# Optimization experiments

Hardware: AMD Instinct MI355X
Metric: run time of the kernel (lower is better)

Reference implementation:

```python
import jax, jax.numpy as jnp
import numpy as np

N = 50000      # nodes per graph
E = 1600000    # edges per graph
D_IN = 128
D_HID = 128
D_OUT = 128
D_GF = 128
N_LAYERS = 3   # input->hid, hid->hid (hidden_layer=1), hid->out


def setup_inputs() -> dict:
    key = jax.random.key(0)
    ks = jax.random.split(key, 24)
    inp = {
        "feat_p": jax.random.normal(ks[0], (N, D_IN), jnp.float32),
        "src_p": jax.random.randint(ks[1], (E,), 0, N, jnp.int32),
        "dst_p": jax.random.randint(ks[2], (E,), 0, N, jnp.int32),
        "feat_s": jax.random.normal(ks[3], (N, D_IN), jnp.float32),
        "src_s": jax.random.randint(ks[4], (E,), 0, N, jnp.int32),
        "dst_s": jax.random.randint(ks[5], (E,), 0, N, jnp.int32),
    }
    dims = [(D_IN, D_HID), (D_HID, D_HID), (D_HID, D_OUT)]
    for i, (di, do) in enumerate(dims):
        inp[f"W{i}"] = jax.random.normal(ks[6 + 2 * i], (di, do), jnp.float32) * 0.05
        inp[f"b{i}"] = jnp.zeros((do,), jnp.float32)
    inp["Wr"] = jax.random.normal(ks[14], (D_OUT, D_GF), jnp.float32) * 0.05
    inp["br"] = jnp.zeros((D_GF,), jnp.float32)
    inp["Wm1"] = jax.random.normal(ks[15], (2 * D_GF, D_GF), jnp.float32) * 0.05
    inp["bm1"] = jnp.zeros((D_GF,), jnp.float32)
    inp["Wm2"] = jax.random.normal(ks[16], (D_GF, 1), jnp.float32) * 0.05
    inp["bm2"] = jnp.zeros((1,), jnp.float32)
    return inp


def _gcn_stack(feat, src, dst, layers):
    """Stacked GCN: mean over incoming messages, then linear.
    NOTE: the original SingleGCN never applies its ReLU (bug preserved)."""
    n = feat.shape[0]
    deg = jax.ops.segment_sum(jnp.ones_like(src, feat.dtype), dst, num_segments=n)
    inv_deg = (1.0 / jnp.maximum(deg, 1.0))[:, None]  # [N,1]
    h = feat
    for W, b in layers:
        msg = h[src]                                           # [E,d] gather
        agg = jax.ops.segment_sum(msg, dst, num_segments=n)    # [N,d] scatter-add
        h = (agg * inv_deg) @ W + b                            # mean + linear
    return h


def reference(feat_p, src_p, dst_p, feat_s, src_s, dst_s,
              W0, b0, W1, b1, W2, b2, Wr, br, Wm1, bm1, Wm2, bm2):
    layers = [(W0, b0), (W1, b1), (W2, b2)]
    h_p = _gcn_stack(feat_p, src_p, dst_p, layers)
    h_s = _gcn_stack(feat_s, src_s, dst_s, layers)
    # ReadOut: mean over nodes -> linear -> sigmoid
    g_p = jax.nn.sigmoid(jnp.mean(h_p, axis=0) @ Wr + br)  # [D_GF]
    g_s = jax.nn.sigmoid(jnp.mean(h_s, axis=0) @ Wr + br)
    # Match: concat -> linear -> linear -> sigmoid
    c = jnp.concatenate([g_p, g_s], axis=-1)               # [2*D_GF]
    d = (c @ Wm1 + bm1) @ Wm2 + bm2                        # [1]
    return jax.nn.sigmoid(d)
```

## Files before the change

kernel.cpp:

```cpp
#include <hip/hip_runtime.h>
#include <math.h>

#define D 128
#define BSH 9
#define NPB 512
#define SLOT 128
#define STCAP 6252
#define NBB 256
#define NBKT_MAX 128
#define SB 8
#define CPS (NBB / SB)


__global__ __launch_bounds__(512) void bin_kernel(
        const int* __restrict__ src_p, const int* __restrict__ dst_p,
        const int* __restrict__ src_s, const int* __restrict__ dst_s,
        int* __restrict__ sbins, unsigned short* __restrict__ dbins,
        unsigned* __restrict__ cnt_s, unsigned* __restrict__ cnt_d,
        int E, int nbkt) {
    const int g = blockIdx.y, b = blockIdx.x;
    const int* src = g ? src_s : src_p;
    const int* dst = g ? dst_s : dst_p;
    int* sb = sbins + (size_t)g * nbkt * NBB * SLOT;
    unsigned short* db = dbins + (size_t)g * nbkt * NBB * SLOT;
    unsigned* csp = cnt_s + (size_t)g * nbkt * NBB;
    unsigned* cdp = cnt_d + (size_t)g * nbkt * NBB;

    __shared__ int sstage[STCAP];
    __shared__ unsigned short dstage[STCAP];
    __shared__ unsigned hist_s[NBKT_MAX], hist_d[NBKT_MAX];
    __shared__ unsigned offs_s[NBKT_MAX], offs_d[NBKT_MAX];
    __shared__ unsigned lcur_s[NBKT_MAX], lcur_d[NBKT_MAX];

    const int tid = threadIdx.x;
    const int wv = tid >> 6, lane = tid & 63;
    for (int i = tid; i < NBKT_MAX; i += 512) { hist_s[i] = 0u; hist_d[i] = 0u; }
    __syncthreads();

    const int e0 = b * STCAP;
    const int e1 = min(e0 + STCAP, E);
    const int efull = e0 + ((e1 - e0) & ~3);

    for (int e = e0 + tid * 4; e + 4 <= e1; e += 512 * 4) {
        int4 s4 = *(const int4*)(src + e);
        int4 d4 = *(const int4*)(dst + e);
        atomicAdd(&hist_s[s4.x >> BSH], 1u);
        atomicAdd(&hist_s[s4.y >> BSH], 1u);
        atomicAdd(&hist_s[s4.z >> BSH], 1u);
        atomicAdd(&hist_s[s4.w >> BSH], 1u);
        atomicAdd(&hist_d[d4.x >> BSH], 1u);
        atomicAdd(&hist_d[d4.y >> BSH], 1u);
        atomicAdd(&hist_d[d4.z >> BSH], 1u);
        atomicAdd(&hist_d[d4.w >> BSH], 1u);
    }
    for (int e = efull + tid; e < e1; e += 512) {
        atomicAdd(&hist_s[src[e] >> BSH], 1u);
        atomicAdd(&hist_d[dst[e] >> BSH], 1u);
    }
    __syncthreads();

    if (wv == 0 || wv == 1) {
        const unsigned* h = (wv == 0) ? hist_s : hist_d;
        unsigned* o = (wv == 0) ? offs_s : offs_d;
        unsigned* lc = (wv == 0) ? lcur_s : lcur_d;
        unsigned a = (2 * lane < nbkt) ? h[2 * lane] : 0u;
        unsigned bb = (2 * lane + 1 < nbkt) ? h[2 * lane + 1] : 0u;
        unsigned v = a + bb;
        for (int d2 = 1; d2 < 64; d2 <<= 1) {
            unsigned t = __shfl_up(v, d2);
            if (lane >= d2) v += t;
        }
        unsigned ex = v - (a + bb);
        if (2 * lane < nbkt) { o[2 * lane] = ex; lc[2 * lane] = ex; }
        if (2 * lane + 1 < nbkt) { o[2 * lane + 1] = ex + a; lc[2 * lane + 1] = ex + a; }
    }
    __syncthreads();

    for (int e = e0 + tid * 4; e + 4 <= e1; e += 512 * 4) {
        int4 s4 = *(const int4*)(src + e);
        int4 d4 = *(const int4*)(dst + e);
        int sv[4] = {s4.x, s4.y, s4.z, s4.w};
        int dv[4] = {d4.x, d4.y, d4.z, d4.w};
        #pragma unroll
        for (int k = 0; k < 4; ++k) {
            unsigned p = atomicAdd(&lcur_s[sv[k] >> BSH], 1u);
            sstage[p] = ((sv[k] & (NPB - 1)) << 17) | dv[k];
            unsigned pd = atomicAdd(&lcur_d[dv[k] >> BSH], 1u);
            dstage[pd] = (unsigned short)(dv[k] & (NPB - 1));
        }
    }
    for (int e = efull + tid; e < e1; e += 512) {
        int s = src[e], d2 = dst[e];
        unsigned p = atomicAdd(&lcur_s[s >> BSH], 1u);
        sstage[p] = ((s & (NPB - 1)) << 17) | d2;
        unsigned pd = atomicAdd(&lcur_d[d2 >> BSH], 1u);
        dstage[pd] = (unsigned short)(d2 & (NPB - 1));
    }
    __syncthreads();

    for (int q = wv; q < nbkt; q += 8) {
        unsigned cs = min(hist_s[q], (unsigned)SLOT);
        unsigned os = offs_s[q];
        int* dp = sb + ((size_t)q * NBB + b) * SLOT;
        for (unsigned i = lane; i < cs; i += 64) dp[i] = sstage[os + i];
        unsigned cd = min(hist_d[q], (unsigned)SLOT);
        unsigned od = offs_d[q];
        unsigned short* ddp = db + ((size_t)q * NBB + b) * SLOT;
        for (unsigned i = lane; i < cd; i += 64) ddp[i] = dstage[od + i];
        if (lane == 0) { csp[q * NBB + b] = cs; cdp[q * NBB + b] = cd; }
    }
}

__global__ __launch_bounds__(256) void deg_part(
        const unsigned short* __restrict__ dbins, const unsigned* __restrict__ cnt_d,
        float* __restrict__ partials, int nbkt) {
    const int s = blockIdx.x, q = blockIdx.y, g = blockIdx.z;
    const unsigned short* dq = dbins + ((size_t)(g * nbkt + q) * NBB + s * CPS) * SLOT;
    const unsigned* cq = cnt_d + (size_t)(g * nbkt + q) * NBB + s * CPS;
    const int tid = threadIdx.x, wv = tid >> 6;
    __shared__ float bl[4][NPB];
    __shared__ unsigned lcnt[CPS];
    if (tid < CPS) lcnt[tid] = cq[tid];
    for (int i = tid; i < 4 * NPB; i += 256) ((float*)bl)[i] = 0.f;
    __syncthreads();
    float* mybl = bl[wv];
    const ushort4* d4 = (const ushort4*)dq;
    const int total = CPS * (SLOT / 4);
    for (int i = tid; i < total; i += 256) {
        int lim = (int)lcnt[i >> 5] - ((i & 31) << 2);
        if (lim <= 0) continue;
        ushort4 v = d4[i];
        atomicAdd(&mybl[v.x], 1.f);
        if (lim > 1) atomicAdd(&mybl[v.y], 1.f);
        if (lim > 2) atomicAdd(&mybl[v.z], 1.f);
        if (lim > 3) atomicAdd(&mybl[v.w], 1.f);
    }
    __syncthreads();
    float* pp = partials + (((size_t)(g * nbkt + q)) * SB + s) * NPB;
    for (int i = tid; i < NPB; i += 256)
        pp[i] = bl[0][i] + bl[1][i] + bl[2][i] + bl[3][i];
}

__global__ __launch_bounds__(512) void deg_combine(
        const float* __restrict__ partials, float* __restrict__ inv,
        float* __restrict__ zbase, int zcount, int N, int nbkt) {
    const int q = blockIdx.x, g = blockIdx.y;
    const int tid = threadIdx.x;
    if (q == 0 && g == 0)
        for (int i = tid; i < zcount; i += 512) zbase[i] = 0.f;
    const float* pp = partials + ((size_t)(g * nbkt + q)) * SB * NPB;
    float t = 0.f;
    #pragma unroll
    for (int s = 0; s < SB; ++s) t += pp[s * NPB + tid];
    const int node = q * NPB + tid;
    if (node < N) inv[(size_t)g * N + node] = 1.0f / fmaxf(t, 1.0f);
}

__global__ __launch_bounds__(256) void part_scan(
        const int* __restrict__ sbins, const unsigned* __restrict__ cnt_s,
        const float* __restrict__ w, float* __restrict__ partials,
        int N, int nbkt) {
    const int s = blockIdx.x, q = blockIdx.y, g = blockIdx.z;
    const int* sq = sbins + ((size_t)(g * nbkt + q) * NBB + s * CPS) * SLOT;
    const unsigned* cq = cnt_s + (size_t)(g * nbkt + q) * NBB + s * CPS;
    const float* wg = w + (size_t)g * N;
    const int tid = threadIdx.x, wv = tid >> 6;
    __shared__ float bl[4][NPB];
    __shared__ unsigned lcnt[CPS];
    if (tid < CPS) lcnt[tid] = cq[tid];
    for (int i = tid; i < 4 * NPB; i += 256) ((float*)bl)[i] = 0.f;
    __syncthreads();
    float* mybl = bl[wv];
    const int4* s4 = (const int4*)sq;
    const int total = CPS * (SLOT / 4);
    for (int i = tid; i < total; i += 256) {
        int lim = (int)lcnt[i >> 5] - ((i & 31) << 2);
        if (lim <= 0) continue;
        int4 v = s4[i];
        int iy = (lim > 1) ? (v.y & 0x1FFFF) : 0;
        int iz = (lim > 2) ? (v.z & 0x1FFFF) : 0;
        int iw = (lim > 3) ? (v.w & 0x1FFFF) : 0;
        float a = wg[v.x & 0x1FFFF];
        float b2 = wg[iy];
        float c2 = wg[iz];
        float d2 = wg[iw];
        atomicAdd(&mybl[((unsigned)v.x) >> 17], a);
        if (lim > 1) atomicAdd(&mybl[((unsigned)v.y) >> 17], b2);
        if (lim > 2) atomicAdd(&mybl[((unsigned)v.z) >> 17], c2);
        if (lim > 3) atomicAdd(&mybl[((unsigned)v.w) >> 17], d2);
    }
    __syncthreads();
    float* pp = partials + (((size_t)(g * nbkt + q)) * SB + s) * NPB;
    for (int i = tid; i < NPB; i += 256)
        pp[i] = bl[0][i] + bl[1][i] + bl[2][i] + bl[3][i];
}

__global__ __launch_bounds__(512) void prop_combine(
        const float* __restrict__ partials, const float* __restrict__ inv,
        float* __restrict__ out_w, float* __restrict__ sums, int s_idx,
        int N, int nbkt, float scale) {
    const int q = blockIdx.x, g = blockIdx.y;
    const int tid = threadIdx.x;
    const float* pp = partials + ((size_t)(g * nbkt + q)) * SB * NPB;
    float t = 0.f;
    #pragma unroll
    for (int s = 0; s < SB; ++s) t += pp[s * NPB + tid];
    const float u = t * scale;
    const int node = q * NPB + tid;
    const bool valid = node < N;
    if (valid) {
        size_t off = (size_t)g * N + node;
        out_w[off] = u * inv[off];
    }
    __shared__ float red[NPB];
    red[tid] = valid ? u : 0.f;
    __syncthreads();
    for (int st = 256; st > 0; st >>= 1) {
        if (tid < st) red[tid] += red[tid + st];
        __syncthreads();
    }
    if (tid == 0 && red[0] != 0.f) atomicAdd(&sums[g * 2 + s_idx], red[0]);
}

__global__ __launch_bounds__(512) void feat_combine(
        const float* __restrict__ partials,
        const float* __restrict__ feat_p, const float* __restrict__ feat_s,
        float* __restrict__ fpart2, int N, int nbkt) {
    const int r = blockIdx.x, q = blockIdx.y, g = blockIdx.z;
    const int tid = threadIdx.x;
    __shared__ float red[256];
    __shared__ float accb[512];
    const float* pp = partials + ((size_t)(g * nbkt + q)) * SB * NPB + r * 256;
    const int base = q * NPB + r * 256;
    if (tid < 256) {
        float t = 0.f;
        #pragma unroll
        for (int s = 0; s < SB; ++s) t += pp[s * NPB + tid];
        red[tid] = (base + tid < N) ? t : 0.f;
    }
    __syncthreads();
    const float* feat = g ? feat_s : feat_p;
    const int j = tid & 127, rg = tid >> 7;
    int rmax = N - base;
    rmax = (rmax < 0) ? 0 : ((rmax > 256) ? 256 : rmax);
    const int rstart = rg * 64;
    const int rend = min(rstart + 64, rmax);
    float acc = 0.f;
    for (int row = rstart; row < rend; ++row)
        acc += red[row] * feat[(size_t)(base + row) * D + j];
    accb[rg * 128 + j] = acc;
    __syncthreads();
    if (rg == 0) {
        float tot = accb[j] + accb[128 + j] + accb[256 + j] + accb[384 + j];
        if (tot != 0.f)
            atomicAdd(&fpart2[((size_t)g * 16 + (q & 15)) * D + j], tot);
    }
}

__global__ __launch_bounds__(512) void final_kernel(
        const float* __restrict__ fpart2,
        const float* __restrict__ sums,
        const float* __restrict__ W0, const float* __restrict__ b0,
        const float* __restrict__ W1, const float* __restrict__ b1,
        const float* __restrict__ W2, const float* __restrict__ b2,
        const float* __restrict__ Wr, const float* __restrict__ br,
        const float* __restrict__ Wm1, const float* __restrict__ bm1,
        const float* __restrict__ Wm2, const float* __restrict__ bm2,
        float* __restrict__ out) {
    __shared__ float x[128];
    __shared__ float part[4][128];
    __shared__ float rvec[256];
    __shared__ float Avec[128], Bvec[128];
    __shared__ float gv[256];
    const int tid = threadIdx.x;
    const int j = tid & 127;
    const int h = tid >> 7;

    auto mv128 = [&](const float* __restrict__ W, float* __restrict__ buf) {
        float p = 0.f;
        const float* Wp = W + (size_t)(h * 32) * 128 + j;
        #pragma unroll
        for (int i = 0; i < 32; ++i) p += buf[h * 32 + i] * Wp[(size_t)i * 128];
        part[h][j] = p;
        __syncthreads();
        if (h == 0) buf[j] = part[0][j] + part[1][j] + part[2][j] + part[3][j];
        __syncthreads();
    };

    if (tid < 256) {
        int g = tid >> 7;
        const float* fp = fpart2 + (size_t)g * 2048 + (tid & 127);
        float rv = 0.f;
        #pragma unroll
        for (int b = 0; b < 16; ++b) rv += fp[(size_t)b * 128];
        rvec[tid] = rv;
    }
    __syncthreads();

    if (tid < 128) x[tid] = b0[tid];
    __syncthreads();
    mv128(W1, x);
    mv128(W2, x);
    if (tid < 128) Avec[tid] = x[tid];
    __syncthreads();
    if (tid < 128) x[tid] = b1[tid];
    __syncthreads();
    mv128(W2, x);
    if (tid < 128) Bvec[tid] = x[tid];
    __syncthreads();

    for (int g = 0; g < 2; ++g) {
        const float s1 = sums[g * 2 + 0];
        const float s2 = sums[g * 2 + 1];
        if (tid < 128) x[tid] = rvec[g * 128 + tid];
        __syncthreads();
        mv128(W0, x);
        mv128(W1, x);
        mv128(W2, x);
        if (tid < 128) x[tid] += s2 * Avec[tid] + s1 * Bvec[tid] + b2[tid];
        __syncthreads();
        mv128(Wr, x);
        if (tid < 128) gv[g * 128 + tid] = 1.0f / (1.0f + expf(-(x[tid] + br[tid])));
        __syncthreads();
    }

    {
        float p = 0.f;
        const float* Wp = Wm1 + (size_t)(h * 64) * 128 + j;
        #pragma unroll
        for (int i = 0; i < 64; ++i) p += gv[h * 64 + i] * Wp[(size_t)i * 128];
        part[h][j] = p;
        __syncthreads();
        if (h == 0)
            part[0][j] = (part[0][j] + part[1][j] + part[2][j] + part[3][j] + bm1[j]) * Wm2[j];
        __syncthreads();
        if (tid < 64) part[0][tid] += part[0][tid + 64];
        __syncthreads();
        if (tid < 32) part[0][tid] += part[0][tid + 32];
        __syncthreads();
        if (tid < 16) part[0][tid] += part[0][tid + 16];
        __syncthreads();
        if (tid < 8) part[0][tid] += part[0][tid + 8];
        __syncthreads();
        if (tid < 4) part[0][tid] += part[0][tid + 4];
        __syncthreads();
        if (tid < 2) part[0][tid] += part[0][tid + 2];
        __syncthreads();
        if (tid == 0) out[0] = 1.0f / (1.0f + expf(-(part[0][0] + part[0][1] + bm2[0])));
    }
}

extern "C" void kernel_launch(void* const* d_in, const int* in_sizes, int n_in,
                              void* d_out, int out_size, void* d_ws, size_t ws_size,
                              hipStream_t stream) {
    const float* feat_p = (const float*)d_in[0];
    const int*   src_p  = (const int*)d_in[1];
    const int*   dst_p  = (const int*)d_in[2];
    const float* feat_s = (const float*)d_in[3];
    const int*   src_s  = (const int*)d_in[4];
    const int*   dst_s  = (const int*)d_in[5];
    const float* W0 = (const float*)d_in[6];
    const float* b0 = (const float*)d_in[7];
    const float* W1 = (const float*)d_in[8];
    const float* b1 = (const float*)d_in[9];
    const float* W2 = (const float*)d_in[10];
    const float* b2 = (const float*)d_in[11];
    const float* Wr = (const float*)d_in[12];
    const float* br = (const float*)d_in[13];
    const float* Wm1 = (const float*)d_in[14];
    const float* bm1 = (const float*)d_in[15];
    const float* Wm2 = (const float*)d_in[16];
    const float* bm2 = (const float*)d_in[17];
    float* out = (float*)d_out;

    const int N = in_sizes[0] / D;
    const int E = in_sizes[1];
    const int N2 = 2 * N;
    const int nbkt = (N + NPB - 1) >> BSH;

    float* ws     = (float*)d_ws;
    float* sums   = ws;
    float* fpart2 = ws + 16;
    float* inv    = fpart2 + 2 * 16 * 128;
    float* w1     = inv + N2;
    float* w2     = w1 + N2;
    float* partials = w2 + N2;
    unsigned* cnt_s = (unsigned*)(partials + (size_t)2 * nbkt * SB * NPB);
    unsigned* cnt_d = cnt_s + (size_t)2 * nbkt * NBB;
    int* sbins    = (int*)(cnt_d + (size_t)2 * nbkt * NBB);
    unsigned short* dbins = (unsigned short*)(sbins + (size_t)2 * nbkt * NBB * SLOT);

    const float u0 = 1.0f / (float)N;
    const int zcount = 16 + 2 * 16 * 128;

    bin_kernel<<<dim3(NBB, 2), 512, 0, stream>>>(src_p, dst_p, src_s, dst_s,
                                                 sbins, dbins, cnt_s, cnt_d,
                                                 E, nbkt);

    deg_part<<<dim3(SB, nbkt, 2), 256, 0, stream>>>(dbins, cnt_d, partials, nbkt);
    deg_combine<<<dim3(nbkt, 2), 512, 0, stream>>>(partials, inv, ws, zcount,
                                                   N, nbkt);

    part_scan<<<dim3(SB, nbkt, 2), 256, 0, stream>>>(sbins, cnt_s, inv,
                                                     partials, N, nbkt);
    prop_combine<<<dim3(nbkt, 2), 512, 0, stream>>>(partials, inv, w1,
                                                    sums, 0, N, nbkt, u0);

    part_scan<<<dim3(SB, nbkt, 2), 256, 0, stream>>>(sbins, cnt_s, w1,
                                                     partials, N, nbkt);
    prop_combine<<<dim3(nbkt, 2), 512, 0, stream>>>(partials, inv, w2,
                                                    sums, 1, N, nbkt, 1.0f);

    part_scan<<<dim3(SB, nbkt, 2), 256, 0, stream>>>(sbins, cnt_s, w2,
                                                     partials, N, nbkt);
    feat_combine<<<dim3(2, nbkt, 2), 512, 0, stream>>>(partials, feat_p, feat_s,
                                                       fpart2, N, nbkt);

    final_kernel<<<1, 512, 0, stream>>>(fpart2, sums, W0, b0, W1, b1, W2, b2,
                                        Wr, br, Wm1, bm1, Wm2, bm2, out);
}
```

Baseline: 300.8 us.

## Split binning by key side, widen scan blocks, parallelize feat and final kernels

The binning kernel now runs separate blocks for src-keyed and dst-keyed binning, doubling grid parallelism and halving shared staging per block. The partial-scan and degree kernels use 512 threads with SB reduced to 4, batching loads ahead of the shared atomics to raise memory-level parallelism. feat_combine is split across 8 row chunks with float4 loads and a tree reduction into 32 accumulator slots. final_kernel processes both graphs concurrently with 1024 threads. The risk is extra passes over src/dst and more global atomics in feat_combine.

```diff
diff --git a/kernel.cpp b/kernel.cpp
--- a/kernel.cpp
+++ b/kernel.cpp
@@ -8,7 +8,7 @@
 #define STCAP 6252
 #define NBB 256
 #define NBKT_MAX 128
-#define SB 8
+#define SB 4
 #define CPS (NBB / SB)
 
 
@@ -18,23 +18,17 @@
         int* __restrict__ sbins, unsigned short* __restrict__ dbins,
         unsigned* __restrict__ cnt_s, unsigned* __restrict__ cnt_d,
         int E, int nbkt) {
-    const int g = blockIdx.y, b = blockIdx.x;
+    const int b = blockIdx.x, side = blockIdx.y, g = blockIdx.z;
     const int* src = g ? src_s : src_p;
     const int* dst = g ? dst_s : dst_p;
-    int* sb = sbins + (size_t)g * nbkt * NBB * SLOT;
-    unsigned short* db = dbins + (size_t)g * nbkt * NBB * SLOT;
-    unsigned* csp = cnt_s + (size_t)g * nbkt * NBB;
-    unsigned* cdp = cnt_d + (size_t)g * nbkt * NBB;
-
-    __shared__ int sstage[STCAP];
-    __shared__ unsigned short dstage[STCAP];
-    __shared__ unsigned hist_s[NBKT_MAX], hist_d[NBKT_MAX];
-    __shared__ unsigned offs_s[NBKT_MAX], offs_d[NBKT_MAX];
-    __shared__ unsigned lcur_s[NBKT_MAX], lcur_d[NBKT_MAX];
+    const int* key = side ? dst : src;
+
+    __shared__ int stage[STCAP];
+    __shared__ unsigned hist[NBKT_MAX], offs[NBKT_MAX], lcur[NBKT_MAX];
 
     const int tid = threadIdx.x;
     const int wv = tid >> 6, lane = tid & 63;
-    for (int i = tid; i < NBKT_MAX; i += 512) { hist_s[i] = 0u; hist_d[i] = 0u; }
+    for (int i = tid; i < NBKT_MAX; i += 512) hist[i] = 0u;
     __syncthreads();
 
     const int e0 = b * STCAP;
@@ -42,103 +36,124 @@
     const int efull = e0 + ((e1 - e0) & ~3);
 
     for (int e = e0 + tid * 4; e + 4 <= e1; e += 512 * 4) {
-        int4 s4 = *(const int4*)(src + e);
-        int4 d4 = *(const int4*)(dst + e);
-        atomicAdd(&hist_s[s4.x >> BSH], 1u);
-        atomicAdd(&hist_s[s4.y >> BSH], 1u);
-        atomicAdd(&hist_s[s4.z >> BSH], 1u);
-        atomicAdd(&hist_s[s4.w >> BSH], 1u);
-        atomicAdd(&hist_d[d4.x >> BSH], 1u);
-        atomicAdd(&hist_d[d4.y >> BSH], 1u);
-        atomicAdd(&hist_d[d4.z >> BSH], 1u);
-        atomicAdd(&hist_d[d4.w >> BSH], 1u);
-    }
-    for (int e = efull + tid; e < e1; e += 512) {
-        atomicAdd(&hist_s[src[e] >> BSH], 1u);
-        atomicAdd(&hist_d[dst[e] >> BSH], 1u);
-    }
-    __syncthreads();
-
-    if (wv == 0 || wv == 1) {
-        const unsigned* h = (wv == 0) ? hist_s : hist_d;
-        unsigned* o = (wv == 0) ? offs_s : offs_d;
-        unsigned* lc = (wv == 0) ? lcur_s : lcur_d;
-        unsigned a = (2 * lane < nbkt) ? h[2 * lane] : 0u;
-        unsigned bb = (2 * lane + 1 < nbkt) ? h[2 * lane + 1] : 0u;
+        int4 k4 = *(const int4*)(key + e);
+        atomicAdd(&hist[k4.x >> BSH], 1u);
+        atomicAdd(&hist[k4.y >> BSH], 1u);
+        atomicAdd(&hist[k4.z >> BSH], 1u);
+        atomicAdd(&hist[k4.w >> BSH], 1u);
+    }
+    for (int e = efull + tid; e < e1; e += 512)
+        atomicAdd(&hist[key[e] >> BSH], 1u);
+    __syncthreads();
+
+    if (wv == 0) {
+        unsigned a = (2 * lane < nbkt) ? hist[2 * lane] : 0u;
+        unsigned bb = (2 * lane + 1 < nbkt) ? hist[2 * lane + 1] : 0u;
         unsigned v = a + bb;
         for (int d2 = 1; d2 < 64; d2 <<= 1) {
             unsigned t = __shfl_up(v, d2);
             if (lane >= d2) v += t;
         }
         unsigned ex = v - (a + bb);
-        if (2 * lane < nbkt) { o[2 * lane] = ex; lc[2 * lane] = ex; }
-        if (2 * lane + 1 < nbkt) { o[2 * lane + 1] = ex + a; lc[2 * lane + 1] = ex + a; }
-    }
-    __syncthreads();
-
-    for (int e = e0 + tid * 4; e + 4 <= e1; e += 512 * 4) {
-        int4 s4 = *(const int4*)(src + e);
-        int4 d4 = *(const int4*)(dst + e);
-        int sv[4] = {s4.x, s4.y, s4.z, s4.w};
-        int dv[4] = {d4.x, d4.y, d4.z, d4.w};
-        #pragma unroll
-        for (int k = 0; k < 4; ++k) {
-            unsigned p = atomicAdd(&lcur_s[sv[k] >> BSH], 1u);
-            sstage[p] = ((sv[k] & (NPB - 1)) << 17) | dv[k];
-            unsigned pd = atomicAdd(&lcur_d[dv[k] >> BSH], 1u);
-            dstage[pd] = (unsigned short)(dv[k] & (NPB - 1));
-        }
-    }
-    for (int e = efull + tid; e < e1; e += 512) {
-        int s = src[e], d2 = dst[e];
-        unsigned p = atomicAdd(&lcur_s[s >> BSH], 1u);
-        sstage[p] = ((s & (NPB - 1)) << 17) | d2;
-        unsigned pd = atomicAdd(&lcur_d[d2 >> BSH], 1u);
-        dstage[pd] = (unsigned short)(d2 & (NPB - 1));
-    }
-    __syncthreads();
-
-    for (int q = wv; q < nbkt; q += 8) {
-        unsigned cs = min(hist_s[q], (unsigned)SLOT);
-        unsigned os = offs_s[q];
-        int* dp = sb + ((size_t)q * NBB + b) * SLOT;
-        for (unsigned i = lane; i < cs; i += 64) dp[i] = sstage[os + i];
-        unsigned cd = min(hist_d[q], (unsigned)SLOT);
-        unsigned od = offs_d[q];
-        unsigned short* ddp = db + ((size_t)q * NBB + b) * SLOT;
-        for (unsigned i = lane; i < cd; i += 64) ddp[i] = dstage[od + i];
-        if (lane == 0) { csp[q * NBB + b] = cs; cdp[q * NBB + b] = cd; }
-    }
-}
-
-__global__ __launch_bounds__(256) void deg_part(
+        if (2 * lane < nbkt) { offs[2 * lane] = ex; lcur[2 * lane] = ex; }
+        if (2 * lane + 1 < nbkt) { offs[2 * lane + 1] = ex + a; lcur[2 * lane + 1] = ex + a; }
+    }
+    __syncthreads();
+
+    if (side == 0) {
+        for (int e = e0 + tid * 4; e + 4 <= e1; e += 512 * 4) {
+            int4 s4 = *(const int4*)(src + e);
+            int4 d4 = *(const int4*)(dst + e);
+            int sv[4] = {s4.x, s4.y, s4.z, s4.w};
+            int dv[4] = {d4.x, d4.y, d4.z, d4.w};
+            #pragma unroll
+            for (int k = 0; k < 4; ++k) {
+                unsigned p = atomicAdd(&lcur[sv[k] >> BSH], 1u);
+                stage[p] = ((sv[k] & (NPB - 1)) << 17) | dv[k];
+            }
+        }
+        for (int e = efull + tid; e < e1; e += 512) {
+            int s = src[e], d2 = dst[e];
+            unsigned p = atomicAdd(&lcur[s >> BSH], 1u);
+            stage[p] = ((s & (NPB - 1)) << 17) | d2;
+        }
+        __syncthreads();
+        int* sb = sbins + (size_t)g * nbkt * NBB * SLOT;
+        unsigned* csp = cnt_s + (size_t)g * nbkt * NBB;
+        for (int q = wv; q < nbkt; q += 8) {
+            unsigned cs = min(hist[q], (unsigned)SLOT);
+            unsigned os = offs[q];
+            int* dp = sb + ((size_t)q * NBB + b) * SLOT;
+            for (unsigned i = lane; i < cs; i += 64) dp[i] = stage[os + i];
+            if (lane == 0) csp[q * NBB + b] = cs;
+        }
+    } else {
+        unsigned short* st = (unsigned short*)stage;
+        for (int e = e0 + tid * 4; e + 4 <= e1; e += 512 * 4) {
+            int4 d4 = *(const int4*)(dst + e);
+            int dv[4] = {d4.x, d4.y, d4.z, d4.w};
+            #pragma unroll
+            for (int k = 0; k < 4; ++k) {
+                unsigned p = atomicAdd(&lcur[dv[k] >> BSH], 1u);
+                st[p] = (unsigned short)(dv[k] & (NPB - 1));
+            }
+        }
+        for (int e = efull + tid; e < e1; e += 512) {
+            int d2 = dst[e];
+            unsigned p = atomicAdd(&lcur[d2 >> BSH], 1u);
+            st[p] = (unsigned short)(d2 & (NPB - 1));
+        }
+        __syncthreads();
+        unsigned short* db = dbins + (size_t)g * nbkt * NBB * SLOT;
+        unsigned* cdp = cnt_d + (size_t)g * nbkt * NBB;
+        for (int q = wv; q < nbkt; q += 8) {
+            unsigned cd = min(hist[q], (unsigned)SLOT);
+            unsigned od = offs[q];
+            unsigned short* ddp = db + ((size_t)q * NBB + b) * SLOT;
+            for (unsigned i = lane; i < cd; i += 64) ddp[i] = st[od + i];
+            if (lane == 0) cdp[q * NBB + b] = cd;
+        }
+    }
+}
+
+__global__ __launch_bounds__(512) void deg_part(
         const unsigned short* __restrict__ dbins, const unsigned* __restrict__ cnt_d,
         float* __restrict__ partials, int nbkt) {
     const int s = blockIdx.x, q = blockIdx.y, g = blockIdx.z;
     const unsigned short* dq = dbins + ((size_t)(g * nbkt + q) * NBB + s * CPS) * SLOT;
     const unsigned* cq = cnt_d + (size_t)(g * nbkt + q) * NBB + s * CPS;
     const int tid = threadIdx.x, wv = tid >> 6;
-    __shared__ float bl[4][NPB];
+    __shared__ float bl[8][NPB];
     __shared__ unsigned lcnt[CPS];
     if (tid < CPS) lcnt[tid] = cq[tid];
-    for (int i = tid; i < 4 * NPB; i += 256) ((float*)bl)[i] = 0.f;
+    for (int i = tid; i < 8 * NPB; i += 512) ((float*)bl)[i] = 0.f;
     __syncthreads();
     float* mybl = bl[wv];
     const ushort4* d4 = (const ushort4*)dq;
-    const int total = CPS * (SLOT / 4);
-    for (int i = tid; i < total; i += 256) {
+    ushort4 v[4]; int limv[4];
+    #pragma unroll
+    for (int it = 0; it < 4; ++it) {
+        int i = it * 512 + tid;
         int lim = (int)lcnt[i >> 5] - ((i & 31) << 2);
-        if (lim <= 0) continue;
-        ushort4 v = d4[i];
-        atomicAdd(&mybl[v.x], 1.f);
-        if (lim > 1) atomicAdd(&mybl[v.y], 1.f);
-        if (lim > 2) atomicAdd(&mybl[v.z], 1.f);
-        if (lim > 3) atomicAdd(&mybl[v.w], 1.f);
+        limv[it] = lim;
+        if (lim > 0) v[it] = d4[i];
+    }
+    #pragma unroll
+    for (int it = 0; it < 4; ++it) {
+        if (limv[it] <= 0) continue;
+        atomicAdd(&mybl[v[it].x], 1.f);
+        if (limv[it] > 1) atomicAdd(&mybl[v[it].y], 1.f);
+        if (limv[it] > 2) atomicAdd(&mybl[v[it].z], 1.f);
+        if (limv[it] > 3) atomicAdd(&mybl[v[it].w], 1.f);
     }
     __syncthreads();
     float* pp = partials + (((size_t)(g * nbkt + q)) * SB + s) * NPB;
-    for (int i = tid; i < NPB; i += 256)
-        pp[i] = bl[0][i] + bl[1][i] + bl[2][i] + bl[3][i];
+    for (int i = tid; i < NPB; i += 512) {
+        float t = 0.f;
+        #pragma unroll
+        for (int r = 0; r < 8; ++r) t += bl[r][i];
+        pp[i] = t;
+    }
 }
 
 __global__ __launch_bounds__(512) void deg_combine(
@@ -156,7 +171,7 @@
     if (node < N) inv[(size_t)g * N + node] = 1.0f / fmaxf(t, 1.0f);
 }
 
-__global__ __launch_bounds__(256) void part_scan(
+__global__ __launch_bounds__(512) void part_scan(
         const int* __restrict__ sbins, const unsigned* __restrict__ cnt_s,
         const float* __restrict__ w, float* __restrict__ partials,
         int N, int nbkt) {
@@ -165,34 +180,46 @@
     const unsigned* cq = cnt_s + (size_t)(g * nbkt + q) * NBB + s * CPS;
     const float* wg = w + (size_t)g * N;
     const int tid = threadIdx.x, wv = tid >> 6;
-    __shared__ float bl[4][NPB];
+    __shared__ float bl[8][NPB];
     __shared__ unsigned lcnt[CPS];
     if (tid < CPS) lcnt[tid] = cq[tid];
-    for (int i = tid; i < 4 * NPB; i += 256) ((float*)bl)[i] = 0.f;
+    for (int i = tid; i < 8 * NPB; i += 512) ((float*)bl)[i] = 0.f;
     __syncthreads();
     float* mybl = bl[wv];
     const int4* s4 = (const int4*)sq;
-    const int total = CPS * (SLOT / 4);
-    for (int i = tid; i < total; i += 256) {
+    int4 v[4]; int limv[4];
+    #pragma unroll
+    for (int it = 0; it < 4; ++it) {
+        int i = it * 512 + tid;
         int lim = (int)lcnt[i >> 5] - ((i & 31) << 2);
-        if (lim <= 0) continue;
-        int4 v = s4[i];
-        int iy = (lim > 1) ? (v.y & 0x1FFFF) : 0;
-        int iz = (lim > 2) ? (v.z & 0x1FFFF) : 0;
-        int iw = (lim > 3) ? (v.w & 0x1FFFF) : 0;
-        float a = wg[v.x & 0x1FFFF];
-        float b2 = wg[iy];
-        float c2 = wg[iz];
-        float d2 = wg[iw];
-        atomicAdd(&mybl[((unsigned)v.x) >> 17], a);
-        if (lim > 1) atomicAdd(&mybl[((unsigned)v.y) >> 17], b2);
-        if (lim > 2) atomicAdd(&mybl[((unsigned)v.z) >> 17], c2);
-        if (lim > 3) atomicAdd(&mybl[((unsigned)v.w) >> 17], d2);
+        limv[it] = lim;
+        if (lim > 0) v[it] = s4[i];
+    }
+    float va[4][4];
+    #pragma unroll
+    for (int it = 0; it < 4; ++it) {
+        if (limv[it] <= 0) continue;
+        va[it][0] = wg[v[it].x & 0x1FFFF];
+        va[it][1] = (limv[it] > 1) ? wg[v[it].y & 0x1FFFF] : 0.f;
+        va[it][2] = (limv[it] > 2) ? wg[v[it].z & 0x1FFFF] : 0.f;
+        va[it][3] = (limv[it] > 3) ? wg[v[it].w & 0x1FFFF] : 0.f;
+    }
+    #pragma unroll
+    for (int it = 0; it < 4; ++it) {
+        if (limv[it] <= 0) continue;
+        atomicAdd(&mybl[((unsigned)v[it].x) >> 17], va[it][0]);
+        if (limv[it] > 1) atomicAdd(&mybl[((unsigned)v[it].y) >> 17], va[it][1]);
+        if (limv[it] > 2) atomicAdd(&mybl[((unsigned)v[it].z) >> 17], va[it][2]);
+        if (limv[it] > 3) atomicAdd(&mybl[((unsigned)v[it].w) >> 17], va[it][3]);
     }
     __syncthreads();
     float* pp = partials + (((size_t)(g * nbkt + q)) * SB + s) * NPB;
-    for (int i = tid; i < NPB; i += 256)
-        pp[i] = bl[0][i] + bl[1][i] + bl[2][i] + bl[3][i];
+    for (int i = tid; i < NPB; i += 512) {
+        float t = 0.f;
+        #pragma unroll
+        for (int r = 0; r < 8; ++r) t += bl[r][i];
+        pp[i] = t;
+    }
 }
 
 __global__ __launch_bounds__(512) void prop_combine(
@@ -228,36 +255,57 @@
         float* __restrict__ fpart2, int N, int nbkt) {
     const int r = blockIdx.x, q = blockIdx.y, g = blockIdx.z;
     const int tid = threadIdx.x;
-    __shared__ float red[256];
-    __shared__ float accb[512];
-    const float* pp = partials + ((size_t)(g * nbkt + q)) * SB * NPB + r * 256;
-    const int base = q * NPB + r * 256;
+    const int base = q * NPB + r * 64;
+    __shared__ float tmp[4][64];
+    __shared__ float red[64];
+    __shared__ float4 sm4[512];
+    const float* pp = partials + ((size_t)(g * nbkt + q)) * SB * NPB + r * 64;
     if (tid < 256) {
-        float t = 0.f;
-        #pragma unroll
-        for (int s = 0; s < SB; ++s) t += pp[s * NPB + tid];
+        int s = tid >> 6, n = tid & 63;
+        tmp[s][n] = pp[(size_t)s * NPB + n];
+    }
+    __syncthreads();
+    if (tid < 64) {
+        float t = tmp[0][tid] + tmp[1][tid] + tmp[2][tid] + tmp[3][tid];
         red[tid] = (base + tid < N) ? t : 0.f;
     }
     __syncthreads();
     const float* feat = g ? feat_s : feat_p;
-    const int j = tid & 127, rg = tid >> 7;
-    int rmax = N - base;
-    rmax = (rmax < 0) ? 0 : ((rmax > 256) ? 256 : rmax);
-    const int rstart = rg * 64;
-    const int rend = min(rstart + 64, rmax);
-    float acc = 0.f;
-    for (int row = rstart; row < rend; ++row)
-        acc += red[row] * feat[(size_t)(base + row) * D + j];
-    accb[rg * 128 + j] = acc;
-    __syncthreads();
-    if (rg == 0) {
-        float tot = accb[j] + accb[128 + j] + accb[256 + j] + accb[384 + j];
-        if (tot != 0.f)
-            atomicAdd(&fpart2[((size_t)g * 16 + (q & 15)) * D + j], tot);
-    }
-}
-
-__global__ __launch_bounds__(512) void final_kernel(
+    const float4* f4 = (const float4*)feat;
+    const int col4 = tid & 31, rg = tid >> 5;
+    float4 acc = make_float4(0.f, 0.f, 0.f, 0.f);
+    #pragma unroll
+    for (int k = 0; k < 4; ++k) {
+        int row = rg * 4 + k;
+        if (base + row < N) {
+            float uu = red[row];
+            float4 fv = f4[(size_t)(base + row) * 32 + col4];
+            acc.x += uu * fv.x; acc.y += uu * fv.y;
+            acc.z += uu * fv.z; acc.w += uu * fv.w;
+        }
+    }
+    sm4[tid] = acc;
+    __syncthreads();
+    for (int st = 8; st > 0; st >>= 1) {
+        if (rg < st) {
+            float4 o = sm4[(rg + st) * 32 + col4];
+            float4 a = sm4[rg * 32 + col4];
+            a.x += o.x; a.y += o.y; a.z += o.z; a.w += o.w;
+            sm4[rg * 32 + col4] = a;
+        }
+        __syncthreads();
+    }
+    if (tid < 32) {
+        float4 t = sm4[tid];
+        float* dstp = fpart2 + ((size_t)g * 32 + ((q * 8 + r) & 31)) * D + tid * 4;
+        atomicAdd(dstp + 0, t.x);
+        atomicAdd(dstp + 1, t.y);
+        atomicAdd(dstp + 2, t.z);
+        atomicAdd(dstp + 3, t.w);
+    }
+}
+
+__global__ __launch_bounds__(1024) void final_kernel(
         const float* __restrict__ fpart2,
         const float* __restrict__ sums,
         const float* __restrict__ W0, const float* __restrict__ b0,
@@ -267,60 +315,63 @@
         const float* __restrict__ Wm1, const float* __restrict__ bm1,
         const float* __restrict__ Wm2, const float* __restrict__ bm2,
         float* __restrict__ out) {
-    __shared__ float x[128];
-    __shared__ float part[4][128];
+    __shared__ float x[2][128];
+    __shared__ float part[2][4][128];
     __shared__ float rvec[256];
     __shared__ float Avec[128], Bvec[128];
     __shared__ float gv[256];
+    __shared__ float m1[128];
     const int tid = threadIdx.x;
     const int j = tid & 127;
-    const int h = tid >> 7;
+    const int h = (tid >> 7) & 3;
+    const int gg = tid >> 9;
 
     auto mv128 = [&](const float* __restrict__ W, float* __restrict__ buf) {
         float p = 0.f;
         const float* Wp = W + (size_t)(h * 32) * 128 + j;
         #pragma unroll
         for (int i = 0; i < 32; ++i) p += buf[h * 32 + i] * Wp[(size_t)i * 128];
-        part[h][j] = p;
-        __syncthreads();
-        if (h == 0) buf[j] = part[0][j] + part[1][j] + part[2][j] + part[3][j];
+        part[gg][h][j] = p;
+        __syncthreads();
+        if (h == 0)
+            buf[j] = part[gg][0][j] + part[gg][1][j] + part[gg][2][j] + part[gg][3][j];
         __syncthreads();
     };
 
     if (tid < 256) {
         int g = tid >> 7;
-        const float* fp = fpart2 + (size_t)g * 2048 + (tid & 127);
+        const float* fp = fpart2 + (size_t)g * 4096 + (tid & 127);
         float rv = 0.f;
         #pragma unroll
-        for (int b = 0; b < 16; ++b) rv += fp[(size_t)b * 128];
+        for (int b = 0; b < 32; ++b) rv += fp[(size_t)b * 128];
         rvec[tid] = rv;
     }
     __syncthreads();
 
-    if (tid < 128) x[tid] = b0[tid];
-    __syncthreads();
-    mv128(W1, x);
-    mv128(W2, x);
-    if (tid < 128) Avec[tid] = x[tid];
-    __syncthreads();
-    if (tid < 128) x[tid] = b1[tid];
-    __syncthreads();
-    mv128(W2, x);
-    if (tid < 128) Bvec[tid] = x[tid];
-    __syncthreads();
-
-    for (int g = 0; g < 2; ++g) {
-        const float s1 = sums[g * 2 + 0];
-        const float s2 = sums[g * 2 + 1];
-        if (tid < 128) x[tid] = rvec[g * 128 + tid];
-        __syncthreads();
-        mv128(W0, x);
-        mv128(W1, x);
-        mv128(W2, x);
-        if (tid < 128) x[tid] += s2 * Avec[tid] + s1 * Bvec[tid] + b2[tid];
-        __syncthreads();
-        mv128(Wr, x);
-        if (tid < 128) gv[g * 128 + tid] = 1.0f / (1.0f + expf(-(x[tid] + br[tid])));
+    if (h == 0) x[gg][j] = b0[j];
+    __syncthreads();
+    mv128(W1, x[gg]);
+    mv128(W2, x[gg]);
+    if (tid < 128) Avec[j] = x[0][j];
+    __syncthreads();
+    if (h == 0) x[gg][j] = b1[j];
+    __syncthreads();
+    mv128(W2, x[gg]);
+    if (tid < 128) Bvec[j] = x[0][j];
+    __syncthreads();
+
+    {
+        const float s1 = sums[gg * 2 + 0];
+        const float s2 = sums[gg * 2 + 1];
+        if (h == 0) x[gg][j] = rvec[gg * 128 + j];
+        __syncthreads();
+        mv128(W0, x[gg]);
+        mv128(W1, x[gg]);
+        mv128(W2, x[gg]);
+        if (h == 0) x[gg][j] += s2 * Avec[j] + s1 * Bvec[j] + b2[j];
+        __syncthreads();
+        mv128(Wr, x[gg]);
+        if (h == 0) gv[gg * 128 + j] = 1.0f / (1.0f + expf(-(x[gg][j] + br[j])));
         __syncthreads();
     }
 
@@ -329,24 +380,25 @@
         const float* Wp = Wm1 + (size_t)(h * 64) * 128 + j;
         #pragma unroll
         for (int i = 0; i < 64; ++i) p += gv[h * 64 + i] * Wp[(size_t)i * 128];
-        part[h][j] = p;
-        __syncthreads();
-        if (h == 0)
-            part[0][j] = (part[0][j] + part[1][j] + part[2][j] + part[3][j] + bm1[j]) * Wm2[j];
-        __syncthreads();
-        if (tid < 64) part[0][tid] += part[0][tid + 64];
-        __syncthreads();
-        if (tid < 32) part[0][tid] += part[0][tid + 32];
-        __syncthreads();
-        if (tid < 16) part[0][tid] += part[0][tid + 16];
-        __syncthreads();
-        if (tid < 8) part[0][tid] += part[0][tid + 8];
-        __syncthreads();
-        if (tid < 4) part[0][tid] += part[0][tid + 4];
-        __syncthreads();
-        if (tid < 2) part[0][tid] += part[0][tid + 2];
-        __syncthreads();
-        if (tid == 0) out[0] = 1.0f / (1.0f + expf(-(part[0][0] + part[0][1] + bm2[0])));
+        part[gg][h][j] = p;
+        __syncthreads();
+        if (tid < 128)
+            m1[j] = (part[0][0][j] + part[0][1][j] + part[0][2][j] + part[0][3][j]
+                     + bm1[j]) * Wm2[j];
+        __syncthreads();
+        if (tid < 64) m1[tid] += m1[tid + 64];
+        __syncthreads();
+        if (tid < 32) m1[tid] += m1[tid + 32];
+        __syncthreads();
+        if (tid < 16) m1[tid] += m1[tid + 16];
+        __syncthreads();
+        if (tid < 8) m1[tid] += m1[tid + 8];
+        __syncthreads();
+        if (tid < 4) m1[tid] += m1[tid + 4];
+        __syncthreads();
+        if (tid < 2) m1[tid] += m1[tid + 2];
+        __syncthreads();
+        if (tid == 0) out[0] = 1.0f / (1.0f + expf(-(m1[0] + m1[1] + bm2[0])));
     }
 }
 
@@ -381,7 +433,7 @@
     float* ws     = (float*)d_ws;
     float* sums   = ws;
     float* fpart2 = ws + 16;
-    float* inv    = fpart2 + 2 * 16 * 128;
+    float* inv    = fpart2 + 2 * 32 * 128;
     float* w1     = inv + N2;
     float* w2     = w1 + N2;
     float* partials = w2 + N2;
@@ -391,31 +443,31 @@
     unsigned short* dbins = (unsigned short*)(sbins + (size_t)2 * nbkt * NBB * SLOT);
 
     const float u0 = 1.0f / (float)N;
-    const int zcount = 16 + 2 * 16 * 128;
-
-    bin_kernel<<<dim3(NBB, 2), 512, 0, stream>>>(src_p, dst_p, src_s, dst_s,
-                                                 sbins, dbins, cnt_s, cnt_d,
-                                                 E, nbkt);
-
-    deg_part<<<dim3(SB, nbkt, 2), 256, 0, stream>>>(dbins, cnt_d, partials, nbkt);
+    const int zcount = 16 + 2 * 32 * 128;
+
+    bin_kernel<<<dim3(NBB, 2, 2), 512, 0, stream>>>(src_p, dst_p, src_s, dst_s,
+                                                    sbins, dbins, cnt_s, cnt_d,
+                                                    E, nbkt);
+
+    deg_part<<<dim3(SB, nbkt, 2), 512, 0, stream>>>(dbins, cnt_d, partials, nbkt);
     deg_combine<<<dim3(nbkt, 2), 512, 0, stream>>>(partials, inv, ws, zcount,
                                                    N, nbkt);
 
-    part_scan<<<dim3(SB, nbkt, 2), 256, 0, stream>>>(sbins, cnt_s, inv,
+    part_scan<<<dim3(SB, nbkt, 2), 512, 0, stream>>>(sbins, cnt_s, inv,
                                                      partials, N, nbkt);
     prop_combine<<<dim3(nbkt, 2), 512, 0, stream>>>(partials, inv, w1,
                                                     sums, 0, N, nbkt, u0);
 
-    part_scan<<<dim3(SB, nbkt, 2), 256, 0, stream>>>(sbins, cnt_s, w1,
+    part_scan<<<dim3(SB, nbkt, 2), 512, 0, stream>>>(sbins, cnt_s, w1,
                                                      partials, N, nbkt);
     prop_combine<<<dim3(nbkt, 2), 512, 0, stream>>>(partials, inv, w2,
                                                     sums, 1, N, nbkt, 1.0f);
 
-    part_scan<<<dim3(SB, nbkt, 2), 256, 0, stream>>>(sbins, cnt_s, w2,
+    part_scan<<<dim3(SB, nbkt, 2), 512, 0, stream>>>(sbins, cnt_s, w2,
                                                      partials, N, nbkt);
-    feat_combine<<<dim3(2, nbkt, 2), 512, 0, stream>>>(partials, feat_p, feat_s,
+    feat_combine<<<dim3(8, nbkt, 2), 512, 0, stream>>>(partials, feat_p, feat_s,
                                                        fpart2, N, nbkt);
 
-    final_kernel<<<1, 512, 0, stream>>>(fpart2, sums, W0, b0, W1, b1, W2, b2,
-                                        Wr, br, Wm1, bm1, Wm2, bm2, out);
-}
+    final_kernel<<<1, 1024, 0, stream>>>(fpart2, sums, W0, b0, W1, b1, W2, b2,
+                                         Wr, br, Wm1, bm1, Wm2, bm2, out);
+}
```

After: 292.6 us. 2.7% less time.
